# Kernel tuning notes

Measured on AMD Instinct MI355X. Metric: run time of the kernel, lower is better.

The kernel has to match this reference:

```python
import jax, jax.numpy as jnp
import numpy as np

B, Q, F, D, H = 16384, 1024, 2, 5, 4  # batch, n_qubits, n_features, depth, heads


def setup_inputs() -> dict:
    key = jax.random.key(0)
    ks = iter(jax.random.split(key, 16))
    def rnd(shape, s=0.02):
        return jax.random.normal(next(ks), shape, dtype=jnp.float32) * s
    return {
        "x": jax.random.normal(next(ks), (B, F), dtype=jnp.float32),
        # amplitude_encoder: Linear(F,4Q) -> LN -> GELU -> Linear(4Q,2Q) -> LN -> Tanh -> Linear(2Q,Q)
        "amp_W1": rnd((4 * Q, F)), "amp_b1": jnp.zeros((4 * Q,), jnp.float32),
        "amp_g1": jnp.ones((4 * Q,), jnp.float32), "amp_be1": jnp.zeros((4 * Q,), jnp.float32),
        "amp_W2": rnd((2 * Q, 4 * Q)), "amp_b2": jnp.zeros((2 * Q,), jnp.float32),
        "amp_g2": jnp.ones((2 * Q,), jnp.float32), "amp_be2": jnp.zeros((2 * Q,), jnp.float32),
        "amp_W3": rnd((Q, 2 * Q)), "amp_b3": jnp.zeros((Q,), jnp.float32),
        # phase_encoder: Linear(F,2Q) -> LN -> SiLU -> Linear(2Q,Q) -> Tanh
        "ph_W1": rnd((2 * Q, F)), "ph_b1": jnp.zeros((2 * Q,), jnp.float32),
        "ph_g1": jnp.ones((2 * Q,), jnp.float32), "ph_be1": jnp.zeros((2 * Q,), jnp.float32),
        "ph_W2": rnd((Q, 2 * Q)), "ph_b2": jnp.zeros((Q,), jnp.float32),
        # rotation parameters (depth, Q, 3); only the last depth slice survives the overwrite loop
        "rot_freq": jax.random.normal(next(ks), (D, Q, 3), dtype=jnp.float32),
        "rot_phase": jax.random.normal(next(ks), (D, Q, 3), dtype=jnp.float32),
        # MultiheadAttention(Q, 4 heads)
        "attn_in_w": rnd((3 * Q, Q)), "attn_in_b": jnp.zeros((3 * Q,), jnp.float32),
        "attn_out_w": rnd((Q, Q)), "attn_out_b": jnp.zeros((Q,), jnp.float32),
    }


def _ln(x, g, b):
    m = jnp.mean(x, -1, keepdims=True)
    v = jnp.mean((x - m) ** 2, -1, keepdims=True)
    return (x - m) * jax.lax.rsqrt(v + 1e-5) * g + b


def reference(x, amp_W1, amp_b1, amp_g1, amp_be1, amp_W2, amp_b2, amp_g2, amp_be2,
              amp_W3, amp_b3, ph_W1, ph_b1, ph_g1, ph_be1, ph_W2, ph_b2,
              rot_freq, rot_phase, attn_in_w, attn_in_b, attn_out_w, attn_out_b):
    # amplitude encoder (Dropout is identity in eval mode)
    h = jax.nn.gelu(_ln(x @ amp_W1.T + amp_b1, amp_g1, amp_be1), approximate=False)
    h = jnp.tanh(_ln(h @ amp_W2.T + amp_b2, amp_g2, amp_be2))
    amp = h @ amp_W3.T + amp_b3                      # (B, Q)
    # phase encoder
    p = jax.nn.silu(_ln(x @ ph_W1.T + ph_b1, ph_g1, ph_be1))
    phase = jnp.tanh(p @ ph_W2.T + ph_b2)            # (B, Q)
    # multiscale conv branch: n_features=2 < min kernel size 3 => skipped, combined_conv = 0
    # depth loop overwrites quantum_state each iteration => only depth index D-1 matters
    rx = jnp.sin(amp * rot_freq[-1, :, 0] + rot_phase[-1, :, 0])
    ry = jnp.cos(phase * rot_freq[-1, :, 1] + rot_phase[-1, :, 1])
    rz = jnp.broadcast_to(jnp.tanh(rot_phase[-1, :, 2]), rx.shape)  # tanh(0*f + p)
    qs = (rx + ry + rz) / 3.0                        # (B, Q)
    # MultiheadAttention with seq_len == 1: softmax over a single key is exactly 1,
    # so attended output == V projection regardless of Q/K.
    qkv = qs @ attn_in_w.T + attn_in_b               # (B, 3Q)
    v = qkv[:, 2 * Q:]                               # (B, Q)
    return v @ attn_out_w.T + attn_out_b
```

## Files before the change

kernel.cpp:

```cpp
#include <hip/hip_runtime.h>

using bf16x8 = __attribute__((ext_vector_type(8))) __bf16;
using u16x8  = __attribute__((ext_vector_type(8))) unsigned short;
using f32x4  = __attribute__((ext_vector_type(4))) float;

__device__ __forceinline__ unsigned short f2bf(float f){
  unsigned int u = __float_as_uint(f);
  u += 0x7fffu + ((u >> 16) & 1u);
  return (unsigned short)(u >> 16);
}
__device__ __forceinline__ float bf2f(unsigned short h){
  return __uint_as_float(((unsigned int)h) << 16);
}

__global__ __launch_bounds__(256) void cvt_bf16(const float* __restrict__ s,
                                                unsigned short* __restrict__ d, int n){
  int i = blockIdx.x * 256 + threadIdx.x;
  if (i < n) d[i] = f2bf(s[i]);
}

__global__ __launch_bounds__(256) void front_amp_kernel(
    const float* __restrict__ x,
    const float* __restrict__ W1, const float* __restrict__ b1,
    const float* __restrict__ g1, const float* __restrict__ be1,
    unsigned short* __restrict__ h)
{
  __shared__ float red[256];
  __shared__ float red2[256];
  __shared__ float s_mean, s_inv;
  const int row = blockIdx.x;
  const int tid = threadIdx.x;
  const float x0 = x[row * 2 + 0];
  const float x1 = x[row * 2 + 1];

  const f32x4* W4 = (const f32x4*)(W1 + (size_t)tid * 32);
  float va[16];
  float sum = 0.f, sq = 0.f;
#pragma unroll
  for (int i4 = 0; i4 < 4; i4++){
    f32x4 b4 = *(const f32x4*)(b1 + tid * 16 + i4 * 4);
    f32x4 wa = W4[i4 * 2], wb = W4[i4 * 2 + 1];
    float v0 = x0 * wa[0] + x1 * wa[1] + b4[0];
    float v1 = x0 * wa[2] + x1 * wa[3] + b4[1];
    float v2 = x0 * wb[0] + x1 * wb[1] + b4[2];
    float v3 = x0 * wb[2] + x1 * wb[3] + b4[3];
    va[i4*4+0] = v0; va[i4*4+1] = v1; va[i4*4+2] = v2; va[i4*4+3] = v3;
    sum += v0 + v1 + v2 + v3;
    sq  += v0*v0 + v1*v1 + v2*v2 + v3*v3;
  }
  red[tid] = sum; red2[tid] = sq; __syncthreads();
  for (int s = 128; s > 0; s >>= 1){
    if (tid < s){ red[tid] += red[tid + s]; red2[tid] += red2[tid + s]; }
    __syncthreads();
  }
  if (tid == 0){
    float m = red[0] * (1.0f / 4096.0f);
    float v = red2[0] * (1.0f / 4096.0f) - m * m;
    s_mean = m; s_inv = rsqrtf(v + 1e-5f);
  }
  __syncthreads();
  float mean = s_mean, inv = s_inv;
#pragma unroll
  for (int i8 = 0; i8 < 2; i8++){
    f32x4 ga = *(const f32x4*)(g1  + tid * 16 + i8 * 8);
    f32x4 gb = *(const f32x4*)(g1  + tid * 16 + i8 * 8 + 4);
    f32x4 ba = *(const f32x4*)(be1 + tid * 16 + i8 * 8);
    f32x4 bb = *(const f32x4*)(be1 + tid * 16 + i8 * 8 + 4);
    u16x8 o;
#pragma unroll
    for (int k = 0; k < 8; k++){
      float gk = (k < 4) ? ga[k] : gb[k - 4];
      float bk = (k < 4) ? ba[k] : bb[k - 4];
      float y = (va[i8 * 8 + k] - mean) * inv * gk + bk;
      float ge = 0.5f * y * (1.0f + erff(y * 0.70710678118654752f));
      o[k] = f2bf(ge);
    }
    *(u16x8*)&h[(size_t)row * 4096 + tid * 16 + i8 * 8] = o;
  }
}

__global__ __launch_bounds__(256) void front_ph_kernel(
    const float* __restrict__ x,
    const float* __restrict__ W1, const float* __restrict__ b1,
    const float* __restrict__ g1, const float* __restrict__ be1,
    unsigned short* __restrict__ p)
{
  __shared__ float red[256];
  __shared__ float red2[256];
  __shared__ float s_mean, s_inv;
  const int row = blockIdx.x;
  const int tid = threadIdx.x;
  const float x0 = x[row * 2 + 0];
  const float x1 = x[row * 2 + 1];

  const f32x4* W4 = (const f32x4*)(W1 + (size_t)tid * 16);
  float vp[8];
  float sum = 0.f, sq = 0.f;
#pragma unroll
  for (int i4 = 0; i4 < 2; i4++){
    f32x4 b4 = *(const f32x4*)(b1 + tid * 8 + i4 * 4);
    f32x4 wa = W4[i4 * 2], wb = W4[i4 * 2 + 1];
    float v0 = x0 * wa[0] + x1 * wa[1] + b4[0];
    float v1 = x0 * wa[2] + x1 * wa[3] + b4[1];
    float v2 = x0 * wb[0] + x1 * wb[1] + b4[2];
    float v3 = x0 * wb[2] + x1 * wb[3] + b4[3];
    vp[i4*4+0] = v0; vp[i4*4+1] = v1; vp[i4*4+2] = v2; vp[i4*4+3] = v3;
    sum += v0 + v1 + v2 + v3;
    sq  += v0*v0 + v1*v1 + v2*v2 + v3*v3;
  }
  red[tid] = sum; red2[tid] = sq; __syncthreads();
  for (int s = 128; s > 0; s >>= 1){
    if (tid < s){ red[tid] += red[tid + s]; red2[tid] += red2[tid + s]; }
    __syncthreads();
  }
  if (tid == 0){
    float m = red[0] * (1.0f / 2048.0f);
    float v = red2[0] * (1.0f / 2048.0f) - m * m;
    s_mean = m; s_inv = rsqrtf(v + 1e-5f);
  }
  __syncthreads();
  float mean = s_mean, inv = s_inv;
  {
    f32x4 ga = *(const f32x4*)(g1  + tid * 8);
    f32x4 gb = *(const f32x4*)(g1  + tid * 8 + 4);
    f32x4 ba = *(const f32x4*)(be1 + tid * 8);
    f32x4 bb = *(const f32x4*)(be1 + tid * 8 + 4);
    u16x8 o;
#pragma unroll
    for (int k = 0; k < 8; k++){
      float gk = (k < 4) ? ga[k] : gb[k - 4];
      float bk = (k < 4) ? ba[k] : bb[k - 4];
      float y = (vp[k] - mean) * inv * gk + bk;
      float si = y / (1.0f + expf(-y));
      o[k] = f2bf(si);
    }
    *(u16x8*)&p[(size_t)row * 2048 + tid * 8] = o;
  }
}

__global__ __launch_bounds__(256) void ln_tanh_kernel(
    unsigned short* __restrict__ c, const float* __restrict__ g,
    const float* __restrict__ be)
{
  __shared__ float red[256];
  __shared__ float red2[256];
  __shared__ float s_mean, s_inv;
  const size_t base = (size_t)blockIdx.x * 2048;
  const int tid = threadIdx.x;
  u16x8 cv = *(const u16x8*)&c[base + tid * 8];
  float v[8];
  float sum = 0.f, sq = 0.f;
#pragma unroll
  for (int k = 0; k < 8; k++){
    float t = bf2f(cv[k]);
    v[k] = t; sum += t; sq += t * t;
  }
  red[tid] = sum; red2[tid] = sq; __syncthreads();
  for (int s = 128; s > 0; s >>= 1){
    if (tid < s){ red[tid] += red[tid + s]; red2[tid] += red2[tid + s]; }
    __syncthreads();
  }
  if (tid == 0){
    float m = red[0] * (1.0f / 2048.0f);
    float vv = red2[0] * (1.0f / 2048.0f) - m * m;
    s_mean = m; s_inv = rsqrtf(vv + 1e-5f);
  }
  __syncthreads();
  float mean = s_mean, inv = s_inv;
  {
    f32x4 ga = *(const f32x4*)(g  + tid * 8);
    f32x4 gb = *(const f32x4*)(g  + tid * 8 + 4);
    f32x4 ba = *(const f32x4*)(be + tid * 8);
    f32x4 bb = *(const f32x4*)(be + tid * 8 + 4);
    u16x8 o;
#pragma unroll
    for (int k = 0; k < 8; k++){
      float gk = (k < 4) ? ga[k] : gb[k - 4];
      float bk = (k < 4) ? ba[k] : bb[k - 4];
      float y = (v[k] - mean) * inv * gk + bk;
      o[k] = f2bf(tanhf(y));
    }
    *(u16x8*)&c[base + tid * 8] = o;
  }
}


#define WAITV4() asm volatile("s_waitcnt vmcnt(4)" ::: "memory")
#define WAITV8() asm volatile("s_waitcnt vmcnt(8)" ::: "memory")
#define WAITV0() asm volatile("s_waitcnt vmcnt(0)" ::: "memory")

template<int EPI>
__global__ __launch_bounds__(512, 2) void gemm_bt(
    const unsigned short* __restrict__ A, const unsigned short* __restrict__ B,
    void* __restrict__ outp, int M, int N, int K, int nT,
    const float* __restrict__ bias,
    const float* __restrict__ aux0, const float* __restrict__ aux1,
    const unsigned short* __restrict__ aux2)
{
  __shared__ __align__(16) char smem_raw[131072];
  unsigned short* S = (unsigned short*)smem_raw;

  const int tid  = threadIdx.x;
  const int wave = tid >> 6, lane = tid & 63;
  const int wm = wave >> 1, wn = wave & 1;
  const int lm = lane & 15, lq = lane >> 4;

  int lid = blockIdx.x;
  {
    const int nwg = gridDim.x;
    if ((nwg & 7) == 0) lid = (lid & 7) * (nwg >> 3) + (lid >> 3);
  }
  const int m0 = (lid / nT) * 256, n0 = (lid % nT) * 256;

  f32x4 acc[4][8];
#pragma unroll
  for (int i = 0; i < 4; i++)
#pragma unroll
    for (int j = 0; j < 8; j++) acc[i][j] = (f32x4){0.f, 0.f, 0.f, 0.f};

  const int lr = lane >> 2;
  const int lc = (((lane & 3) ^ ((lr >> 1) & 3)) << 3);
  const unsigned short* gA = A + (size_t)(m0 + wave * 32 + lr) * K + lc;
  const unsigned short* gB = B + (size_t)(n0 + wave * 32 + lr) * K + lc;
  const size_t rowK16 = (size_t)16 * K;

  auto stage = [&](int buf){
    unsigned short* lA = S + buf * 16384 + wave * 1024;
    unsigned short* lB = lA + 8192;
    __builtin_amdgcn_global_load_lds(
        (const __attribute__((address_space(1))) void*)gA,
        (__attribute__((address_space(3))) void*)lA, 16, 0, 0);
    __builtin_amdgcn_global_load_lds(
        (const __attribute__((address_space(1))) void*)(gA + rowK16),
        (__attribute__((address_space(3))) void*)(lA + 512), 16, 0, 0);
    __builtin_amdgcn_global_load_lds(
        (const __attribute__((address_space(1))) void*)gB,
        (__attribute__((address_space(3))) void*)lB, 16, 0, 0);
    __builtin_amdgcn_global_load_lds(
        (const __attribute__((address_space(1))) void*)(gB + rowK16),
        (__attribute__((address_space(3))) void*)(lB + 512), 16, 0, 0);
    gA += 32; gB += 32;
  };

  auto readA = [&](int buf, bf16x8* af){
    const unsigned short* sA = S + buf * 16384;
#pragma unroll
    for (int q = 0; q < 4; q++){
      const int r = wm * 64 + q * 16 + lm;
      af[q] = *(const bf16x8*)&sA[r * 32 + ((lq ^ ((r >> 1) & 3)) << 3)];
    }
  };
  auto readB = [&](int buf, bf16x8* bfr){
    const unsigned short* sB = S + buf * 16384 + 8192;
#pragma unroll
    for (int q = 0; q < 8; q++){
      const int r = wn * 128 + q * 16 + lm;
      bfr[q] = *(const bf16x8*)&sB[r * 32 + ((lq ^ ((r >> 1) & 3)) << 3)];
    }
  };

  auto mfmaAll = [&](const bf16x8* af, const bf16x8* bfr){
    __builtin_amdgcn_s_setprio(1);
#pragma unroll
    for (int i = 0; i < 4; i++)
#pragma unroll
      for (int j = 0; j < 8; j++)
        acc[i][j] = __builtin_amdgcn_mfma_f32_16x16x32_bf16(af[i], bfr[j], acc[i][j], 0, 0, 0);
    __builtin_amdgcn_s_setprio(0);
  };

  const int nTk = K >> 5;
  bf16x8 af[4], bfA[8], bfB[8];
  stage(0); stage(1); stage(2);
  WAITV8();
  __builtin_amdgcn_s_barrier();
  readB(0, bfA);
  for (int t = 0; t < nTk; t += 2){
    if (t + 2 < nTk) WAITV4(); else WAITV0();
    __builtin_amdgcn_s_barrier();
    if (t + 3 < nTk) stage((t + 3) & 3);
    readB((t + 1) & 3, bfB);
    readA(t & 3, af);
    mfmaAll(af, bfA);
    if (t + 2 < nTk){
      if (t + 3 < nTk) WAITV4(); else WAITV0();
    }
    __builtin_amdgcn_s_barrier();
    if (t + 4 < nTk) stage((t + 4) & 3);
    if (t + 2 < nTk) readB((t + 2) & 3, bfA);
    readA((t + 1) & 3, af);
    mfmaAll(af, bfB);
  }

  __syncthreads();
  float* ew = (float*)smem_raw + wave * 2112;

#pragma unroll
  for (int i = 0; i < 4; i++){
#pragma unroll
    for (int j = 0; j < 8; j++){
      const int col = n0 + wn * 128 + j * 16 + lm;
      float bcol = bias[col];
      float f0 = 0.f, p0 = 0.f, rzv = 0.f;
      if constexpr (EPI == 1){
        f0 = aux0[3 * col]; p0 = aux1[3 * col]; rzv = tanhf(aux1[3 * col + 2]);
      }
      if constexpr (EPI == 2){
        f0 = aux0[3 * col + 1]; p0 = aux1[3 * col + 1];
      }
#pragma unroll
      for (int r = 0; r < 4; r++){
        const float val = acc[i][j][r];
        float pre;
        if constexpr (EPI == 0 || EPI == 3)      pre = val + bcol;
        else if constexpr (EPI == 1)             pre = sinf((val + bcol) * f0 + p0) + rzv;
        else                                     pre = cosf(tanhf(val + bcol) * f0 + p0);
        ew[(lq * 4 + r) * 132 + j * 16 + lm] = pre;
      }
    }
    if constexpr (EPI != 3){
#pragma unroll
      for (int s = 0; s < 4; s++){
        const int lrow = 4 * s + lq;
        const int grow = m0 + wm * 64 + i * 16 + lrow;
        const float* src = ew + lrow * 132 + lm * 8;
        f32x4 v0 = *(const f32x4*)(src);
        f32x4 v1 = *(const f32x4*)(src + 4);
        const size_t gidx = (size_t)grow * N + n0 + wn * 128 + lm * 8;
        u16x8 o;
        if constexpr (EPI == 1){
          u16x8 ry8 = *(const u16x8*)&aux2[gidx];
#pragma unroll
          for (int t = 0; t < 4; t++){
            o[t]     = f2bf((v0[t] + bf2f(ry8[t]))     * (1.0f / 3.0f));
            o[t + 4] = f2bf((v1[t] + bf2f(ry8[t + 4])) * (1.0f / 3.0f));
          }
        } else {
#pragma unroll
          for (int t = 0; t < 4; t++){
            o[t] = f2bf(v0[t]); o[t + 4] = f2bf(v1[t]);
          }
        }
        *(u16x8*)&((unsigned short*)outp)[gidx] = o;
      }
    } else {
#pragma unroll
      for (int s = 0; s < 8; s++){
        const int lrow = 2 * s + (lane >> 5);
        const int grow = m0 + wm * 64 + i * 16 + lrow;
        const int lcol = (lane & 31) * 4;
        f32x4 v = *(const f32x4*)(ew + lrow * 132 + lcol);
        *(f32x4*)&((float*)outp)[(size_t)grow * N + n0 + wn * 128 + lcol] = v;
      }
    }
  }
}

extern "C" void kernel_launch(void* const* d_in, const int* in_sizes, int n_in,
                              void* d_out, int out_size, void* d_ws, size_t ws_size,
                              hipStream_t stream)
{
  const float* x    = (const float*)d_in[0];
  const float* aW1  = (const float*)d_in[1];
  const float* ab1  = (const float*)d_in[2];
  const float* ag1  = (const float*)d_in[3];
  const float* abe1 = (const float*)d_in[4];
  const float* aW2  = (const float*)d_in[5];
  const float* ab2  = (const float*)d_in[6];
  const float* ag2  = (const float*)d_in[7];
  const float* abe2 = (const float*)d_in[8];
  const float* aW3  = (const float*)d_in[9];
  const float* ab3  = (const float*)d_in[10];
  const float* pW1  = (const float*)d_in[11];
  const float* pb1  = (const float*)d_in[12];
  const float* pg1  = (const float*)d_in[13];
  const float* pbe1 = (const float*)d_in[14];
  const float* pW2  = (const float*)d_in[15];
  const float* pb2  = (const float*)d_in[16];
  const float* rfreq  = (const float*)d_in[17];
  const float* rphase = (const float*)d_in[18];
  const float* aiw  = (const float*)d_in[19];
  const float* aib  = (const float*)d_in[20];
  const float* aow  = (const float*)d_in[21];
  const float* aob  = (const float*)d_in[22];

  const int B = 16384, Q = 1024;

  char* ws = (char*)d_ws;
  size_t off = 0;
  auto alloc = [&](size_t bytes) -> char* {
    char* ptr = ws + off; off += (bytes + 255) & ~(size_t)255; return ptr;
  };
  unsigned short* Wb2  = (unsigned short*)alloc((size_t)2 * Q * 4 * Q * 2);
  unsigned short* Wb3  = (unsigned short*)alloc((size_t)Q * 2 * Q * 2);
  unsigned short* PWb2 = (unsigned short*)alloc((size_t)Q * 2 * Q * 2);
  unsigned short* WVb  = (unsigned short*)alloc((size_t)Q * Q * 2);
  unsigned short* WOb  = (unsigned short*)alloc((size_t)Q * Q * 2);
  unsigned short* R1   = (unsigned short*)alloc((size_t)B * 4 * Q * 2);
  unsigned short* ry   = (unsigned short*)alloc((size_t)B * Q * 2);

  unsigned short* p  = R1;
  unsigned short* h  = R1;
  unsigned short* qs = R1;
  unsigned short* v  = R1 + (size_t)B * Q;
  unsigned short* c2 = (unsigned short*)d_out;

  cvt_bf16<<<(2*Q*4*Q + 255) / 256, 256, 0, stream>>>(aW2, Wb2, 2*Q*4*Q);
  cvt_bf16<<<(Q*2*Q + 255) / 256, 256, 0, stream>>>(aW3, Wb3, Q*2*Q);
  cvt_bf16<<<(Q*2*Q + 255) / 256, 256, 0, stream>>>(pW2, PWb2, Q*2*Q);
  cvt_bf16<<<(Q*Q + 255) / 256, 256, 0, stream>>>(aiw + (size_t)2*Q*Q, WVb, Q*Q);
  cvt_bf16<<<(Q*Q + 255) / 256, 256, 0, stream>>>(aow, WOb, Q*Q);

  const float* rf4 = rfreq  + (size_t)4 * Q * 3;
  const float* rp4 = rphase + (size_t)4 * Q * 3;

  const int mT = B / 256;
  const int nT1 = 2 * Q / 256;
  const int nTq = Q / 256;

  front_ph_kernel<<<B, 256, 0, stream>>>(x, pW1, pb1, pg1, pbe1, p);
  gemm_bt<2><<<nTq * mT, 512, 0, stream>>>(p, PWb2, ry, B, Q, 2*Q, nTq,
                                           pb2, rf4, rp4, nullptr);

  front_amp_kernel<<<B, 256, 0, stream>>>(x, aW1, ab1, ag1, abe1, h);
  gemm_bt<0><<<nT1 * mT, 512, 0, stream>>>(h, Wb2, c2, B, 2*Q, 4*Q, nT1,
                                           ab2, nullptr, nullptr, nullptr);
  ln_tanh_kernel<<<B, 256, 0, stream>>>(c2, ag2, abe2);

  gemm_bt<1><<<nTq * mT, 512, 0, stream>>>(c2, Wb3, qs, B, Q, 2*Q, nTq,
                                           ab3, rf4, rp4, ry);
  gemm_bt<0><<<nTq * mT, 512, 0, stream>>>(qs, WVb, v, B, Q, Q, nTq,
                                           aib + 2*Q, nullptr, nullptr, nullptr);
  gemm_bt<3><<<nTq * mT, 512, 0, stream>>>(v, WOb, d_out, B, Q, Q, nTq,
                                           aob, nullptr, nullptr, nullptr);
}
```

Baseline: 907.3 us.

## Restructure GEMM main loop into 8-wave ping-pong schedule with 64-wide K tiles

Replaces the 4-buffer 32-wide K pipeline with two 64-wide K buffers, each split into 32-wide halves. Each iteration is split into four phases that interleave LDS reads, MFMA clusters over half of the N fragments, and staged global-to-LDS loads, with barriers between phases. The goal is to overlap memory traffic with MFMA work and to halve B-fragment register use, so that two workgroups per CU can run. In exchange it adds many more barriers and explicit lgkmcnt waits per K step, which may serialize waves.

```diff
diff --git a/kernel.cpp b/kernel.cpp
--- a/kernel.cpp
+++ b/kernel.cpp
@@ -186,8 +186,9 @@
 
 
 #define WAITV4() asm volatile("s_waitcnt vmcnt(4)" ::: "memory")
-#define WAITV8() asm volatile("s_waitcnt vmcnt(8)" ::: "memory")
 #define WAITV0() asm volatile("s_waitcnt vmcnt(0)" ::: "memory")
+#define LGKM0()  do { asm volatile("s_waitcnt lgkmcnt(0)" ::: "memory"); \
+                      __builtin_amdgcn_sched_barrier(0); } while(0)
 
 template<int EPI>
 __global__ __launch_bounds__(512, 2) void gemm_bt(
@@ -224,72 +225,90 @@
   const unsigned short* gB = B + (size_t)(n0 + wave * 32 + lr) * K + lc;
   const size_t rowK16 = (size_t)16 * K;
 
-  auto stage = [&](int buf){
-    unsigned short* lA = S + buf * 16384 + wave * 1024;
-    unsigned short* lB = lA + 8192;
+  auto stageA = [&](int buf, int kk, int tile){
+    unsigned short* d = S + buf * 32768 + kk * 8192 + wave * 1024;
+    const unsigned short* s = gA + (size_t)tile * 64 + kk * 32;
     __builtin_amdgcn_global_load_lds(
-        (const __attribute__((address_space(1))) void*)gA,
-        (__attribute__((address_space(3))) void*)lA, 16, 0, 0);
+        (const __attribute__((address_space(1))) void*)s,
+        (__attribute__((address_space(3))) void*)d, 16, 0, 0);
     __builtin_amdgcn_global_load_lds(
-        (const __attribute__((address_space(1))) void*)(gA + rowK16),
-        (__attribute__((address_space(3))) void*)(lA + 512), 16, 0, 0);
+        (const __attribute__((address_space(1))) void*)(s + rowK16),
+        (__attribute__((address_space(3))) void*)(d + 512), 16, 0, 0);
+  };
+  auto stageB = [&](int buf, int kk, int tile){
+    unsigned short* d = S + buf * 32768 + 16384 + kk * 8192 + wave * 1024;
+    const unsigned short* s = gB + (size_t)tile * 64 + kk * 32;
     __builtin_amdgcn_global_load_lds(
-        (const __attribute__((address_space(1))) void*)gB,
-        (__attribute__((address_space(3))) void*)lB, 16, 0, 0);
+        (const __attribute__((address_space(1))) void*)s,
+        (__attribute__((address_space(3))) void*)d, 16, 0, 0);
     __builtin_amdgcn_global_load_lds(
-        (const __attribute__((address_space(1))) void*)(gB + rowK16),
-        (__attribute__((address_space(3))) void*)(lB + 512), 16, 0, 0);
-    gA += 32; gB += 32;
-  };
-
-  auto readA = [&](int buf, bf16x8* af){
-    const unsigned short* sA = S + buf * 16384;
+        (const __attribute__((address_space(1))) void*)(s + rowK16),
+        (__attribute__((address_space(3))) void*)(d + 512), 16, 0, 0);
+  };
+
+  auto readA4 = [&](int buf, int kk, bf16x8* af){
+    const unsigned short* sA = S + buf * 32768 + kk * 8192;
 #pragma unroll
     for (int q = 0; q < 4; q++){
       const int r = wm * 64 + q * 16 + lm;
       af[q] = *(const bf16x8*)&sA[r * 32 + ((lq ^ ((r >> 1) & 3)) << 3)];
     }
   };
-  auto readB = [&](int buf, bf16x8* bfr){
-    const unsigned short* sB = S + buf * 16384 + 8192;
-#pragma unroll
-    for (int q = 0; q < 8; q++){
-      const int r = wn * 128 + q * 16 + lm;
-      bfr[q] = *(const bf16x8*)&sB[r * 32 + ((lq ^ ((r >> 1) & 3)) << 3)];
-    }
-  };
-
-  auto mfmaAll = [&](const bf16x8* af, const bf16x8* bfr){
+  auto readB4 = [&](int buf, int kk, int jh, bf16x8* bf){
+    const unsigned short* sB = S + buf * 32768 + 16384 + kk * 8192;
+#pragma unroll
+    for (int q = 0; q < 4; q++){
+      const int r = wn * 128 + jh * 64 + q * 16 + lm;
+      bf[q] = *(const bf16x8*)&sB[r * 32 + ((lq ^ ((r >> 1) & 3)) << 3)];
+    }
+  };
+
+  auto mfma16 = [&](int jh, const bf16x8* af, const bf16x8* bf){
     __builtin_amdgcn_s_setprio(1);
 #pragma unroll
     for (int i = 0; i < 4; i++)
 #pragma unroll
-      for (int j = 0; j < 8; j++)
-        acc[i][j] = __builtin_amdgcn_mfma_f32_16x16x32_bf16(af[i], bfr[j], acc[i][j], 0, 0, 0);
+      for (int q = 0; q < 4; q++)
+        acc[i][jh * 4 + q] =
+            __builtin_amdgcn_mfma_f32_16x16x32_bf16(af[i], bf[q], acc[i][jh * 4 + q], 0, 0, 0);
     __builtin_amdgcn_s_setprio(0);
   };
 
-  const int nTk = K >> 5;
-  bf16x8 af[4], bfA[8], bfB[8];
-  stage(0); stage(1); stage(2);
-  WAITV8();
+  const int nT64 = K >> 6;
+  bf16x8 af[4], bf[4];
+
+  stageA(0, 0, 0); stageB(0, 0, 0); stageA(0, 1, 0); stageB(0, 1, 0);
+  stageA(1, 0, 1); stageB(1, 0, 1);
+  WAITV4();
   __builtin_amdgcn_s_barrier();
-  readB(0, bfA);
-  for (int t = 0; t < nTk; t += 2){
-    if (t + 2 < nTk) WAITV4(); else WAITV0();
-    __builtin_amdgcn_s_barrier();
-    if (t + 3 < nTk) stage((t + 3) & 3);
-    readB((t + 1) & 3, bfB);
-    readA(t & 3, af);
-    mfmaAll(af, bfA);
-    if (t + 2 < nTk){
-      if (t + 3 < nTk) WAITV4(); else WAITV0();
-    }
-    __builtin_amdgcn_s_barrier();
-    if (t + 4 < nTk) stage((t + 4) & 3);
-    if (t + 2 < nTk) readB((t + 2) & 3, bfA);
-    readA((t + 1) & 3, af);
-    mfmaAll(af, bfB);
+
+  for (int t = 0; t < nT64; ++t){
+    const int c = t & 1;
+    readA4(c, 0, af); readB4(c, 0, 0, bf);
+    if (t + 1 < nT64) stageA(c ^ 1, 1, t + 1);
+    __builtin_amdgcn_s_barrier();
+    LGKM0();
+    mfma16(0, af, bf);
+    __builtin_amdgcn_s_barrier();
+    readB4(c, 0, 1, bf);
+    if (t + 1 < nT64) stageB(c ^ 1, 1, t + 1);
+    __builtin_amdgcn_s_barrier();
+    LGKM0();
+    mfma16(1, af, bf);
+    __builtin_amdgcn_s_barrier();
+    readA4(c, 1, af); readB4(c, 1, 0, bf);
+    if (t + 2 < nT64) stageA(c, 0, t + 2);
+    __builtin_amdgcn_s_barrier();
+    LGKM0();
+    mfma16(0, af, bf);
+    __builtin_amdgcn_s_barrier();
+    readB4(c, 1, 1, bf);
+    if (t + 2 < nT64) stageB(c, 0, t + 2);
+    __builtin_amdgcn_s_barrier();
+    LGKM0();
+    mfma16(1, af, bf);
+    if (t + 2 < nT64) WAITV4(); else WAITV0();
+    __builtin_amdgcn_s_barrier();
   }
 
   __syncthreads();
```

Result: no change. 904.4 us (-0.3%).
